# Performance work log

Measured on AMD Instinct MI355X. Metric: run time of the kernel, lower is better.

## Reference

```python
import jax, jax.numpy as jnp
import numpy as np

NUM_LEVELS = 16
FEATURES_PER_LEVEL = 2
LOG2_HASHMAP_SIZE = 19
BASE_RES = 16
FINEST_RES = 2048
N_POINTS = 2097152

_growth = np.exp((np.log(FINEST_RES) - np.log(BASE_RES)) / (NUM_LEVELS - 1))
RESOLUTIONS = np.floor(BASE_RES * _growth ** np.arange(NUM_LEVELS)).astype(np.int64)  # (L,)
TABLE_SIZES = np.minimum(RESOLUTIONS ** 3, 2 ** LOG2_HASHMAP_SIZE).astype(np.int32)   # (L,)
MAX_TABLE_SIZE = 2 ** LOG2_HASHMAP_SIZE

P1, P2, P3 = 73856093, 19349663, 83492791  # spatial hash primes


def setup_inputs() -> dict:
    key = jax.random.key(0)
    k1, k2 = jax.random.split(key)
    coordinates = jax.random.uniform(k1, (N_POINTS, 3), dtype=jnp.float32)
    # keras 'uniform' initializer = U(-0.05, 0.05); tables stacked & zero-padded to max size
    hash_tables = jax.random.uniform(
        k2, (NUM_LEVELS, MAX_TABLE_SIZE, FEATURES_PER_LEVEL),
        minval=-0.05, maxval=0.05, dtype=jnp.float32)
    return {"coordinates": coordinates, "hash_tables": hash_tables}


def reference(coordinates, hash_tables):
    batch_shape = coordinates.shape[:-1]
    coords = coordinates.reshape(-1, 3)  # (N, 3)
    res = jnp.asarray(RESOLUTIONS.astype(np.float32))          # (L,)
    sizes = jnp.asarray(TABLE_SIZES)                            # (L,) int32
    # all levels at once: (L, N, 3)
    grid = jnp.floor(coords[None, :, :] * res[:, None, None]).astype(jnp.int32)
    x, y, t = grid[..., 0], grid[..., 1], grid[..., 2]
    h = (x * np.int32(P1)) ^ (y * np.int32(P2)) ^ (t * np.int32(P3))  # int32 wraparound, like TF
    idx = jnp.abs(h) % sizes[:, None]                           # (L, N)
    feats = jnp.take_along_axis(hash_tables, idx[:, :, None], axis=1)  # (L, N, F)
    out = jnp.transpose(feats, (1, 0, 2)).reshape(coords.shape[0], NUM_LEVELS * FEATURES_PER_LEVEL)
    return out.reshape(*batch_shape, NUM_LEVELS * FEATURES_PER_LEVEL)
```

## Files before the change

### kernel.cpp

```cpp
#include <hip/hip_runtime.h>
#include <stdint.h>


#define TPB 256

typedef float vfloat4 __attribute__((ext_vector_type(4)));
typedef float vfloat2 __attribute__((ext_vector_type(2)));

__device__ __forceinline__ uint32_t hash_idx(float cx, float cy, float cz,
                                             int resi, int siz)
{
    const float rf = (float)resi;
    const int x = (int)floorf(cx * rf);
    const int y = (int)floorf(cy * rf);
    const int z = (int)floorf(cz * rf);
    const uint32_t h = (uint32_t)x * 73856093u
                     ^ (uint32_t)y * 19349663u
                     ^ (uint32_t)z * 83492791u;
    const int32_t hs = (int32_t)h;
    if (siz == (1 << 19)) {
        const uint32_t a = (hs < 0) ? (0u - h) : h;
        return a & 0x7FFFFu;
    } else {
        int32_t a = (hs < 0) ? (int32_t)(0u - h) : hs;
        int32_t r = a % siz;
        if (r < 0) r += siz;
        return (uint32_t)r;
    }
}

#define RESI_LIST {16, 22, 30, 42, 58, 80, 111, 153, \
                   212, 294, 406, 561, 776, 1072, 1482, 2048}
#define SIZ_LIST  {4096, 10648, 27000, 74088, 195112, 512000, \
                   524288, 524288, 524288, 524288, 524288, \
                   524288, 524288, 524288, 524288, 524288}

template<int LV>
__global__ __launch_bounds__(TPB) void hashenc_gather_lv(
    const float* __restrict__ coords,
    const float* __restrict__ tables,
    float2* __restrict__ ws,
    int npts)
{
    constexpr int RESI[16] = RESI_LIST;
    constexpr int SIZ[16] = SIZ_LIST;

    const int t = threadIdx.x;
    const long long base = (long long)blockIdx.x * 2048;
    const float* tab = tables + ((size_t)LV << 20);

    vfloat2 g[8];
#pragma unroll
    for (int j = 0; j < 8; ++j) {
        const long long p = base + j * 256 + t;
        const float cx = coords[3 * p + 0];
        const float cy = coords[3 * p + 1];
        const float cz = coords[3 * p + 2];
        const uint32_t idx = hash_idx(cx, cy, cz, RESI[LV], SIZ[LV]);
        g[j] = *reinterpret_cast<const vfloat2*>(tab + ((size_t)idx << 1));
    }
    float2* wl = ws + (size_t)(LV - 5) * npts + base;
#pragma unroll
    for (int j = 0; j < 8; ++j)
        __builtin_nontemporal_store(g[j],
            reinterpret_cast<vfloat2*>(wl + j * 256 + t));
}

__global__ __launch_bounds__(TPB) void hashenc_transpose_fused(
    const float* __restrict__ coords,
    const float* __restrict__ tables,
    const float2* __restrict__ ws,
    float* __restrict__ out,
    int npts)
{
    constexpr int RESI[16] = RESI_LIST;
    constexpr int SIZ[16] = SIZ_LIST;

    __shared__ float buf[128 * 33];

    const int t = threadIdx.x;
    const long long pbase = (long long)blockIdx.x * TPB;
    const long long p = pbase + t;

    const float cx = coords[3 * p + 0];
    const float cy = coords[3 * p + 1];
    const float cz = coords[3 * p + 2];

    vfloat2 feat[16];
#pragma unroll
    for (int l = 0; l < 5; ++l) {
        const uint32_t idx = hash_idx(cx, cy, cz, RESI[l], SIZ[l]);
        feat[l] = *reinterpret_cast<const vfloat2*>(
            tables + ((size_t)l << 20) + ((size_t)idx << 1));
    }
#pragma unroll
    for (int l = 5; l < 16; ++l)
        feat[l] = __builtin_nontemporal_load(
            reinterpret_cast<const vfloat2*>(ws + (size_t)(l - 5) * npts + p));

    float* oblk = out + pbase * 32;
#pragma unroll
    for (int h = 0; h < 2; ++h) {
        if ((t >> 7) == h) {
            const int r = t & 127;
#pragma unroll
            for (int l = 0; l < 16; ++l) {
                buf[r * 33 + 2 * l + 0] = feat[l].x;
                buf[r * 33 + 2 * l + 1] = feat[l].y;
            }
        }
        __syncthreads();
#pragma unroll
        for (int k = 0; k < 4; ++k) {
            const int f = k * 1024 + t * 4;
            const int row = f >> 5;
            const int col = f & 31;
            const vfloat4 v = *reinterpret_cast<const vfloat4*>(&buf[row * 33 + col]);
            __builtin_nontemporal_store(v,
                reinterpret_cast<vfloat4*>(&oblk[(long long)h * 4096 + f]));
        }
        __syncthreads();
    }
}

__global__ __launch_bounds__(TPB) void hashenc_kernel(
    const float* __restrict__ coords,
    const float* __restrict__ tables,
    float* __restrict__ out,
    int npts)
{
    constexpr int RESI[16] = RESI_LIST;
    constexpr int SIZ[16] = SIZ_LIST;

    __shared__ float buf[128 * 33];

    const int t = threadIdx.x;
    const long long pbase = (long long)blockIdx.x * TPB;
    const long long p = pbase + t;

    const float cx = coords[3 * p + 0];
    const float cy = coords[3 * p + 1];
    const float cz = coords[3 * p + 2];

    float2 feat[16];
#pragma unroll
    for (int l = 0; l < 16; ++l) {
        const uint32_t idx = hash_idx(cx, cy, cz, RESI[l], SIZ[l]);
        feat[l] = *reinterpret_cast<const float2*>(
            tables + ((size_t)l << 20) + ((size_t)idx << 1));
    }

    float* oblk = out + pbase * 32;
#pragma unroll
    for (int h = 0; h < 2; ++h) {
        if ((t >> 7) == h) {
            const int r = t & 127;
#pragma unroll
            for (int l = 0; l < 16; ++l) {
                buf[r * 33 + 2 * l + 0] = feat[l].x;
                buf[r * 33 + 2 * l + 1] = feat[l].y;
            }
        }
        __syncthreads();
#pragma unroll
        for (int k = 0; k < 4; ++k) {
            const int f = k * 1024 + t * 4;
            const int row = f >> 5;
            const int col = f & 31;
            const vfloat4 v = *reinterpret_cast<const vfloat4*>(&buf[row * 33 + col]);
            __builtin_nontemporal_store(v,
                reinterpret_cast<vfloat4*>(&oblk[(long long)h * 4096 + f]));
        }
        __syncthreads();
    }
}

extern "C" void kernel_launch(void* const* d_in, const int* in_sizes, int n_in,
                              void* d_out, int out_size, void* d_ws, size_t ws_size,
                              hipStream_t stream)
{
    const float* coords = (const float*)d_in[0];
    const float* tables = (const float*)d_in[1];
    float* out = (float*)d_out;
    const int npts = in_sizes[0] / 3;

    const size_t need = (size_t)11 * (size_t)npts * sizeof(float2);
    if (ws_size >= need && (npts % 2048) == 0) {
        float2* ws = (float2*)d_ws;
        const dim3 g(npts / 2048), b(TPB);
        hipLaunchKernelGGL((hashenc_gather_lv<5>),  g, b, 0, stream, coords, tables, ws, npts);
        hipLaunchKernelGGL((hashenc_gather_lv<6>),  g, b, 0, stream, coords, tables, ws, npts);
        hipLaunchKernelGGL((hashenc_gather_lv<7>),  g, b, 0, stream, coords, tables, ws, npts);
        hipLaunchKernelGGL((hashenc_gather_lv<8>),  g, b, 0, stream, coords, tables, ws, npts);
        hipLaunchKernelGGL((hashenc_gather_lv<9>),  g, b, 0, stream, coords, tables, ws, npts);
        hipLaunchKernelGGL((hashenc_gather_lv<10>), g, b, 0, stream, coords, tables, ws, npts);
        hipLaunchKernelGGL((hashenc_gather_lv<11>), g, b, 0, stream, coords, tables, ws, npts);
        hipLaunchKernelGGL((hashenc_gather_lv<12>), g, b, 0, stream, coords, tables, ws, npts);
        hipLaunchKernelGGL((hashenc_gather_lv<13>), g, b, 0, stream, coords, tables, ws, npts);
        hipLaunchKernelGGL((hashenc_gather_lv<14>), g, b, 0, stream, coords, tables, ws, npts);
        hipLaunchKernelGGL((hashenc_gather_lv<15>), g, b, 0, stream, coords, tables, ws, npts);
        hipLaunchKernelGGL(hashenc_transpose_fused, dim3(npts / TPB), b, 0, stream,
                           coords, tables, (const float2*)d_ws, out, npts);
    } else {
        hipLaunchKernelGGL(hashenc_kernel, dim3(npts / TPB), dim3(TPB), 0, stream,
                           coords, tables, out, npts);
    }
}
```

Before: 327.0 us.

## Merge per-level gather launches into one interleaved kernel

```diff
diff --git a/kernel.cpp b/kernel.cpp
--- a/kernel.cpp
+++ b/kernel.cpp
@@ -36,17 +36,16 @@
                    524288, 524288, 524288, 524288, 524288}
 
 template<int LV>
-__global__ __launch_bounds__(TPB) void hashenc_gather_lv(
+__device__ __forceinline__ void gather_body(
     const float* __restrict__ coords,
     const float* __restrict__ tables,
     float2* __restrict__ ws,
-    int npts)
+    int npts, long long pb, int t)
 {
     constexpr int RESI[16] = RESI_LIST;
     constexpr int SIZ[16] = SIZ_LIST;
 
-    const int t = threadIdx.x;
-    const long long base = (long long)blockIdx.x * 2048;
+    const long long base = pb * 2048;
     const float* tab = tables + ((size_t)LV << 20);
 
     vfloat2 g[8];
@@ -66,6 +65,42 @@
             reinterpret_cast<vfloat2*>(wl + j * 256 + t));
 }
 
+__global__ __launch_bounds__(TPB) void hashenc_gather_merged(
+    const float* __restrict__ coords,
+    const float* __restrict__ tables,
+    float2* __restrict__ ws,
+    int npts)
+{
+    const int t = threadIdx.x;
+    const int c = blockIdx.x & 7;
+    const long long k = blockIdx.x >> 3;
+    const long long npb = (long long)npts >> 11;
+
+    if (k < npb) {
+        switch (c) {
+            case 0: gather_body<5>(coords, tables, ws, npts, k, t); break;
+            case 1: gather_body<6>(coords, tables, ws, npts, k, t); break;
+            case 2: gather_body<7>(coords, tables, ws, npts, k, t); break;
+            case 3: gather_body<8>(coords, tables, ws, npts, k, t); break;
+            case 4: gather_body<9>(coords, tables, ws, npts, k, t); break;
+            case 5: gather_body<10>(coords, tables, ws, npts, k, t); break;
+            case 6: gather_body<11>(coords, tables, ws, npts, k, t); break;
+            case 7: gather_body<12>(coords, tables, ws, npts, k, t); break;
+        }
+    } else {
+        const long long per_class = (3 * npb + 7) >> 3;
+        const long long ti = (long long)c * per_class + (k - npb);
+        if (ti < 3 * npb) {
+            const long long pb = ti % npb;
+            switch ((int)(ti / npb)) {
+                case 0: gather_body<13>(coords, tables, ws, npts, pb, t); break;
+                case 1: gather_body<14>(coords, tables, ws, npts, pb, t); break;
+                case 2: gather_body<15>(coords, tables, ws, npts, pb, t); break;
+            }
+        }
+    }
+}
+
 __global__ __launch_bounds__(TPB) void hashenc_transpose_fused(
     const float* __restrict__ coords,
     const float* __restrict__ tables,
@@ -187,18 +222,11 @@
     const size_t need = (size_t)11 * (size_t)npts * sizeof(float2);
     if (ws_size >= need && (npts % 2048) == 0) {
         float2* ws = (float2*)d_ws;
-        const dim3 g(npts / 2048), b(TPB);
-        hipLaunchKernelGGL((hashenc_gather_lv<5>),  g, b, 0, stream, coords, tables, ws, npts);
-        hipLaunchKernelGGL((hashenc_gather_lv<6>),  g, b, 0, stream, coords, tables, ws, npts);
-        hipLaunchKernelGGL((hashenc_gather_lv<7>),  g, b, 0, stream, coords, tables, ws, npts);
-        hipLaunchKernelGGL((hashenc_gather_lv<8>),  g, b, 0, stream, coords, tables, ws, npts);
-        hipLaunchKernelGGL((hashenc_gather_lv<9>),  g, b, 0, stream, coords, tables, ws, npts);
-        hipLaunchKernelGGL((hashenc_gather_lv<10>), g, b, 0, stream, coords, tables, ws, npts);
-        hipLaunchKernelGGL((hashenc_gather_lv<11>), g, b, 0, stream, coords, tables, ws, npts);
-        hipLaunchKernelGGL((hashenc_gather_lv<12>), g, b, 0, stream, coords, tables, ws, npts);
-        hipLaunchKernelGGL((hashenc_gather_lv<13>), g, b, 0, stream, coords, tables, ws, npts);
-        hipLaunchKernelGGL((hashenc_gather_lv<14>), g, b, 0, stream, coords, tables, ws, npts);
-        hipLaunchKernelGGL((hashenc_gather_lv<15>), g, b, 0, stream, coords, tables, ws, npts);
+        const long long npb = npts / 2048;
+        const long long per_class = (3 * npb + 7) / 8;
+        const dim3 g((unsigned)(8 * (npb + per_class))), b(TPB);
+        hipLaunchKernelGGL(hashenc_gather_merged, g, b, 0, stream,
+                           coords, tables, ws, npts);
         hipLaunchKernelGGL(hashenc_transpose_fused, dim3(npts / TPB), b, 0, stream,
                            coords, tables, (const float2*)d_ws, out, npts);
     } else {
```

New measurement: 292.8 us. 1.12x faster.
